# Optimization experiments

Hardware: AMD Instinct MI355X
Metric: run time of the kernel (lower is better)

The kernel has to match this reference:

```python
import jax, jax.numpy as jnp
import numpy as np

H = 2048       # hidden_size
E = 8          # num_experts
K = 2          # top_k
I = 16         # expert bottleneck (intermediate_size)


def setup_inputs() -> dict:
    key = jax.random.key(0)
    k1, k2, k3, k4 = jax.random.split(key, 4)
    B, T = 2, 4096
    x = jax.random.normal(k1, (B, T, H), dtype=jnp.float32)
    # nn.Linear weight layout is (out, in); init scale ~ 1/sqrt(fan_in)
    router_w = jax.random.normal(k2, (E, H), dtype=jnp.float32) / np.sqrt(H)
    down_w = jax.random.normal(k3, (E, I, H), dtype=jnp.float32) / np.sqrt(H)
    up_w = jax.random.normal(k4, (E, H, I), dtype=jnp.float32) / np.sqrt(I)
    return {"x": x, "router_w": router_w, "down_w": down_w, "up_w": up_w}


def reference(x, router_w, down_w, up_w):
    # router
    logits = jnp.einsum('bth,eh->bte', x, router_w)        # [B,T,E]
    weights = jax.nn.softmax(logits, axis=-1)
    top_w, top_idx = jax.lax.top_k(weights, K)             # [B,T,K]
    # gate[b,t,e] = softmax weight if e in top-k else 0 (top-k of softmax
    # values are distinct a.s., so masking == scatter of top_w)
    topk_mask = jnp.sum(jax.nn.one_hot(top_idx, E, dtype=x.dtype), axis=-2)  # [B,T,E]
    gate = weights * topk_mask                              # [B,T,E]
    # dense expert compute on all tokens (matches original's redundant compute)
    h = jnp.einsum('bth,eih->beti', x, down_w)             # [B,E,T,I]
    a = jax.nn.silu(h)
    expert_out = jnp.einsum('beti,ehi->beth', a, up_w)     # [B,E,T,H]
    # masked combine
    out = jnp.einsum('beth,bte->bth', expert_out, gate)    # [B,T,H]
    return out
```

## Files before the change

kernel.cpp:

```cpp
#include <hip/hip_runtime.h>
#include <math.h>

#define HDIM 2048
#define NEXP 8
#define IDIM 16
#define N_EI 128

typedef __attribute__((ext_vector_type(8))) short bf16x8;
typedef __attribute__((ext_vector_type(4))) float f32x4;

static __device__ __forceinline__ short f2bf(float f) {
    union { float f; unsigned u; } v; v.f = f;
    unsigned r = v.u + 0x7fffu + ((v.u >> 16) & 1u);
    return (short)(r >> 16);
}

__global__ __launch_bounds__(256) void prep_kernel(
    const float* __restrict__ x, const float* __restrict__ rw,
    const float* __restrict__ dw, const float* __restrict__ uw,
    float* __restrict__ gate_ws, short* __restrict__ b1p, short* __restrict__ b2p,
    short* __restrict__ x_bf, int T, int routerBlocks, int doXbf)
{
    const int bid = blockIdx.x;
    if (bid < routerBlocks) {
        const int wave = threadIdx.x >> 6, lane = threadIdx.x & 63;
        const int t = bid * 4 + wave;
        const float* __restrict__ xr = x + (size_t)t * HDIM;
        float4 xv[8];
        #pragma unroll
        for (int j = 0; j < 8; ++j) xv[j] = *(const float4*)(xr + j * 256 + lane * 4);

        if (doXbf) {
            #pragma unroll
            for (int j = 0; j < 8; ++j) {
                unsigned lo = ((unsigned short)f2bf(xv[j].x)) | ((unsigned)(unsigned short)f2bf(xv[j].y) << 16);
                unsigned hi = ((unsigned short)f2bf(xv[j].z)) | ((unsigned)(unsigned short)f2bf(xv[j].w) << 16);
                *(uint2*)(x_bf + (size_t)t * HDIM + j * 256 + lane * 4) = make_uint2(lo, hi);
            }
        }

        float accv[NEXP];
        #pragma unroll
        for (int e = 0; e < NEXP; ++e) {
            const float* __restrict__ wr = rw + (size_t)e * HDIM;
            float acc = 0.f;
            #pragma unroll
            for (int j = 0; j < 8; ++j) {
                float4 wv = *(const float4*)(wr + j * 256 + lane * 4);
                acc += xv[j].x * wv.x + xv[j].y * wv.y + xv[j].z * wv.z + xv[j].w * wv.w;
            }
            accv[e] = acc;
        }
        #pragma unroll
        for (int s = 1; s < 64; s <<= 1) {
            #pragma unroll
            for (int e = 0; e < NEXP; ++e) accv[e] += __shfl_xor(accv[e], s);
        }
        if (lane == 0) {
            float m = accv[0];
            #pragma unroll
            for (int e = 1; e < NEXP; ++e) m = fmaxf(m, accv[e]);
            float w[NEXP], ssum = 0.f;
            #pragma unroll
            for (int e = 0; e < NEXP; ++e) { w[e] = expf(accv[e] - m); ssum += w[e]; }
            const float inv = 1.f / ssum;
            #pragma unroll
            for (int e = 0; e < NEXP; ++e) w[e] *= inv;
            int i1 = 0; float w1 = w[0];
            #pragma unroll
            for (int e = 1; e < NEXP; ++e) if (w[e] > w1) { w1 = w[e]; i1 = e; }
            int i2 = -1; float w2 = -1.f;
            #pragma unroll
            for (int e = 0; e < NEXP; ++e) if (e != i1 && w[e] > w2) { w2 = w[e]; i2 = e; }
            #pragma unroll
            for (int e = 0; e < NEXP; ++e)
                gate_ws[(size_t)t * NEXP + e] = (e == i1) ? w1 : ((e == i2) ? w2 : 0.f);
        }
    } else {
        const int id = (bid - routerBlocks) * 256 + threadIdx.x;
        float4 v0, v1;
        short* dst;
        if (id < 32768) {
            const int kb = id >> 7, n = id & 127;
            const float* __restrict__ src = dw + (size_t)n * HDIM + kb * 8;
            v0 = *(const float4*)(src);
            v1 = *(const float4*)(src + 4);
            dst = b1p + (size_t)id * 8;
        } else {
            const int id2 = id - 32768;
            const int k2b = id2 >> 11, h = id2 & 2047;
            const int e = k2b >> 1, i0 = (k2b & 1) * 8;
            const float* __restrict__ src = uw + ((size_t)e * HDIM + h) * IDIM + i0;
            v0 = *(const float4*)(src);
            v1 = *(const float4*)(src + 4);
            dst = b2p + (size_t)id2 * 8;
        }
        bf16x8 p;
        p[0] = f2bf(v0.x); p[1] = f2bf(v0.y); p[2] = f2bf(v0.z); p[3] = f2bf(v0.w);
        p[4] = f2bf(v1.x); p[5] = f2bf(v1.y); p[6] = f2bf(v1.z); p[7] = f2bf(v1.w);
        *(bf16x8*)dst = p;
    }
}

template<bool XBF>
__global__ __launch_bounds__(512) void down_kernel(
    const float* __restrict__ x, const short* __restrict__ x_bf,
    const float* __restrict__ gate_ws, const short* __restrict__ b1p,
    short* __restrict__ a_gl, int T)
{
    __shared__ float h_part[16][132];

    const int tid = threadIdx.x;
    const int w = tid >> 6, l = tid & 63;
    const int c = l & 15;
    const int kblk = l >> 4;
    const int t0 = blockIdx.x * 16;
    const int nq = w & 3, kh = w >> 2;
    const int n0 = nq * 32;

    f32x4 acc0 = {0,0,0,0}, acc1 = {0,0,0,0};
    const float* __restrict__ xr = x + (size_t)(t0 + c) * HDIM;
    const short* __restrict__ xb = x_bf + (size_t)(t0 + c) * HDIM;

    for (int s = 0; s < 32; ++s) {
        const int k0 = kh * 1024 + s * 32;
        const int ka = k0 + kblk * 8;
        bf16x8 xf;
        if (XBF) {
            xf = *(const bf16x8*)(xb + ka);
        } else {
            float4 a0 = *(const float4*)(xr + ka);
            float4 a1 = *(const float4*)(xr + ka + 4);
            xf[0]=f2bf(a0.x); xf[1]=f2bf(a0.y); xf[2]=f2bf(a0.z); xf[3]=f2bf(a0.w);
            xf[4]=f2bf(a1.x); xf[5]=f2bf(a1.y); xf[6]=f2bf(a1.z); xf[7]=f2bf(a1.w);
        }
        const short* __restrict__ bbase = b1p + ((size_t)(k0 >> 3) + kblk) * 1024;
        bf16x8 wf0 = *(const bf16x8*)(bbase + (n0 + c) * 8);
        bf16x8 wf1 = *(const bf16x8*)(bbase + (n0 + 16 + c) * 8);
        acc0 = __builtin_amdgcn_mfma_f32_16x16x32_bf16(wf0, xf, acc0, 0, 0, 0);
        acc1 = __builtin_amdgcn_mfma_f32_16x16x32_bf16(wf1, xf, acc1, 0, 0, 0);
    }

    if (kh == 1) {
        *(f32x4*)&h_part[c][n0 + kblk * 4]      = acc0;
        *(f32x4*)&h_part[c][n0 + 16 + kblk * 4] = acc1;
    }
    __syncthreads();
    if (kh == 0) {
        const f32x4 pa = *(const f32x4*)&h_part[c][n0 + kblk * 4];
        const f32x4 pb = *(const f32x4*)&h_part[c][n0 + 16 + kblk * 4];
        const float g0 = gate_ws[(size_t)(t0 + c) * NEXP + nq * 2];
        const float g1 = gate_ws[(size_t)(t0 + c) * NEXP + nq * 2 + 1];
        short r0[4], r1[4];
        #pragma unroll
        for (int r = 0; r < 4; ++r) {
            const float h0v = acc0[r] + pa[r];
            const float h1v = acc1[r] + pb[r];
            r0[r] = f2bf(h0v / (1.f + expf(-h0v)) * g0);
            r1[r] = f2bf(h1v / (1.f + expf(-h1v)) * g1);
        }
        short* __restrict__ arow = a_gl + (size_t)(t0 + c) * N_EI;
        *(uint2*)(arow + n0 + kblk * 4) =
            make_uint2(((unsigned short)r0[0]) | ((unsigned)(unsigned short)r0[1] << 16),
                       ((unsigned short)r0[2]) | ((unsigned)(unsigned short)r0[3] << 16));
        *(uint2*)(arow + n0 + 16 + kblk * 4) =
            make_uint2(((unsigned short)r1[0]) | ((unsigned)(unsigned short)r1[1] << 16),
                       ((unsigned short)r1[2]) | ((unsigned)(unsigned short)r1[3] << 16));
    }
}

__global__ __launch_bounds__(512) void up_kernel(
    const short* __restrict__ a_gl, const short* __restrict__ b2p,
    float* __restrict__ out, int T)
{
    const int tid = threadIdx.x;
    const int w = tid >> 6, l = tid & 63;
    const int c = l & 15;
    const int kblk = l >> 4;
    const int bid = blockIdx.x;
    const int tgrp = bid >> 1, bh = bid & 1;
    const int th = w >> 2, hq = w & 3;
    const int t0 = tgrp * 32 + th * 16;
    const int h0 = bh * 1024 + hq * 256;

    f32x4 acc[16];
    #pragma unroll
    for (int f = 0; f < 16; ++f) acc[f] = (f32x4){0,0,0,0};

    const short* __restrict__ arow = a_gl + (size_t)(t0 + c) * N_EI;
    for (int s = 0; s < 4; ++s) {
        bf16x8 af = *(const bf16x8*)(arow + s * 32 + kblk * 8);
        const short* __restrict__ bbase = b2p + ((size_t)(s * 4) + kblk) * 16384;
        #pragma unroll
        for (int f = 0; f < 16; ++f) {
            bf16x8 wfr = *(const bf16x8*)(bbase + (size_t)(h0 + f * 16 + c) * 8);
            acc[f] = __builtin_amdgcn_mfma_f32_16x16x32_bf16(wfr, af, acc[f], 0, 0, 0);
        }
    }
    float* __restrict__ orow = out + (size_t)(t0 + c) * HDIM;
    #pragma unroll
    for (int f = 0; f < 16; ++f)
        *(f32x4*)(orow + h0 + f * 16 + kblk * 4) = acc[f];
}

extern "C" void kernel_launch(void* const* d_in, const int* in_sizes, int n_in,
                              void* d_out, int out_size, void* d_ws, size_t ws_size,
                              hipStream_t stream) {
    const float* x  = (const float*)d_in[0];
    const float* rw = (const float*)d_in[1];
    const float* dw = (const float*)d_in[2];
    const float* uw = (const float*)d_in[3];
    float* out = (float*)d_out;
    const int T = in_sizes[0] / HDIM;

    char* wsb = (char*)d_ws;
    float* gate_ws = (float*)wsb;
    short* b1p  = (short*)(wsb + (size_t)T * NEXP * 4);
    short* b2p  = (short*)(wsb + (size_t)T * NEXP * 4 + 524288);
    short* x_bf = (short*)(wsb + (size_t)T * NEXP * 4 + 1048576);
    const size_t xbf_bytes = (size_t)T * HDIM * 2;

    const size_t need_full  = (size_t)T * NEXP * 4 + 1048576 + xbf_bytes + (size_t)T * N_EI * 2;
    const bool use_xbf = (ws_size >= need_full);
    short* a_gl = use_xbf
        ? (short*)(wsb + (size_t)T * NEXP * 4 + 1048576 + xbf_bytes)
        : (short*)(wsb + (size_t)T * NEXP * 4 + 1048576);

    const int routerBlocks = T / 4;
    prep_kernel<<<routerBlocks + 256, 256, 0, stream>>>(
        x, rw, dw, uw, gate_ws, b1p, b2p, x_bf, T, routerBlocks, use_xbf ? 1 : 0);

    if (use_xbf)
        down_kernel<true><<<T / 16, 512, 0, stream>>>(x, x_bf, gate_ws, b1p, a_gl, T);
    else
        down_kernel<false><<<T / 16, 512, 0, stream>>>(x, x_bf, gate_ws, b1p, a_gl, T);

    up_kernel<<<(T / 32) * 2, 512, 0, stream>>>(a_gl, b2p, out, T);
}
```

Baseline: 173.1 us.

## Fuse router logits, softmax and top-k gating into the down-projection kernel

The router dot products are now computed inside the down-projection kernel from the fp32 x values it already loads, so x is read once instead of twice. The separate bf16 copy of x is no longer written, and the gates stay in LDS instead of going through global memory. Weight packing becomes a small standalone kernel. In exchange the down kernel takes extra router-weight loads, LDS reductions and two more barriers, and every block repeats the weight packing work's dependency order.

```diff
diff --git a/kernel.cpp b/kernel.cpp
--- a/kernel.cpp
+++ b/kernel.cpp
@@ -15,100 +15,42 @@
     return (short)(r >> 16);
 }
 
-__global__ __launch_bounds__(256) void prep_kernel(
+__global__ __launch_bounds__(256) void pack_kernel(
+    const float* __restrict__ dw, const float* __restrict__ uw,
+    short* __restrict__ b1p, short* __restrict__ b2p)
+{
+    const int id = blockIdx.x * 256 + threadIdx.x;
+    float4 v0, v1;
+    short* dst;
+    if (id < 32768) {
+        const int kb = id >> 7, n = id & 127;
+        const float* __restrict__ src = dw + (size_t)n * HDIM + kb * 8;
+        v0 = *(const float4*)(src);
+        v1 = *(const float4*)(src + 4);
+        dst = b1p + (size_t)id * 8;
+    } else {
+        const int id2 = id - 32768;
+        const int k2b = id2 >> 11, h = id2 & 2047;
+        const int e = k2b >> 1, i0 = (k2b & 1) * 8;
+        const float* __restrict__ src = uw + ((size_t)e * HDIM + h) * IDIM + i0;
+        v0 = *(const float4*)(src);
+        v1 = *(const float4*)(src + 4);
+        dst = b2p + (size_t)id2 * 8;
+    }
+    bf16x8 p;
+    p[0] = f2bf(v0.x); p[1] = f2bf(v0.y); p[2] = f2bf(v0.z); p[3] = f2bf(v0.w);
+    p[4] = f2bf(v1.x); p[5] = f2bf(v1.y); p[6] = f2bf(v1.z); p[7] = f2bf(v1.w);
+    *(bf16x8*)dst = p;
+}
+
+__global__ __launch_bounds__(512) void downr_kernel(
     const float* __restrict__ x, const float* __restrict__ rw,
-    const float* __restrict__ dw, const float* __restrict__ uw,
-    float* __restrict__ gate_ws, short* __restrict__ b1p, short* __restrict__ b2p,
-    short* __restrict__ x_bf, int T, int routerBlocks, int doXbf)
-{
-    const int bid = blockIdx.x;
-    if (bid < routerBlocks) {
-        const int wave = threadIdx.x >> 6, lane = threadIdx.x & 63;
-        const int t = bid * 4 + wave;
-        const float* __restrict__ xr = x + (size_t)t * HDIM;
-        float4 xv[8];
-        #pragma unroll
-        for (int j = 0; j < 8; ++j) xv[j] = *(const float4*)(xr + j * 256 + lane * 4);
-
-        if (doXbf) {
-            #pragma unroll
-            for (int j = 0; j < 8; ++j) {
-                unsigned lo = ((unsigned short)f2bf(xv[j].x)) | ((unsigned)(unsigned short)f2bf(xv[j].y) << 16);
-                unsigned hi = ((unsigned short)f2bf(xv[j].z)) | ((unsigned)(unsigned short)f2bf(xv[j].w) << 16);
-                *(uint2*)(x_bf + (size_t)t * HDIM + j * 256 + lane * 4) = make_uint2(lo, hi);
-            }
-        }
-
-        float accv[NEXP];
-        #pragma unroll
-        for (int e = 0; e < NEXP; ++e) {
-            const float* __restrict__ wr = rw + (size_t)e * HDIM;
-            float acc = 0.f;
-            #pragma unroll
-            for (int j = 0; j < 8; ++j) {
-                float4 wv = *(const float4*)(wr + j * 256 + lane * 4);
-                acc += xv[j].x * wv.x + xv[j].y * wv.y + xv[j].z * wv.z + xv[j].w * wv.w;
-            }
-            accv[e] = acc;
-        }
-        #pragma unroll
-        for (int s = 1; s < 64; s <<= 1) {
-            #pragma unroll
-            for (int e = 0; e < NEXP; ++e) accv[e] += __shfl_xor(accv[e], s);
-        }
-        if (lane == 0) {
-            float m = accv[0];
-            #pragma unroll
-            for (int e = 1; e < NEXP; ++e) m = fmaxf(m, accv[e]);
-            float w[NEXP], ssum = 0.f;
-            #pragma unroll
-            for (int e = 0; e < NEXP; ++e) { w[e] = expf(accv[e] - m); ssum += w[e]; }
-            const float inv = 1.f / ssum;
-            #pragma unroll
-            for (int e = 0; e < NEXP; ++e) w[e] *= inv;
-            int i1 = 0; float w1 = w[0];
-            #pragma unroll
-            for (int e = 1; e < NEXP; ++e) if (w[e] > w1) { w1 = w[e]; i1 = e; }
-            int i2 = -1; float w2 = -1.f;
-            #pragma unroll
-            for (int e = 0; e < NEXP; ++e) if (e != i1 && w[e] > w2) { w2 = w[e]; i2 = e; }
-            #pragma unroll
-            for (int e = 0; e < NEXP; ++e)
-                gate_ws[(size_t)t * NEXP + e] = (e == i1) ? w1 : ((e == i2) ? w2 : 0.f);
-        }
-    } else {
-        const int id = (bid - routerBlocks) * 256 + threadIdx.x;
-        float4 v0, v1;
-        short* dst;
-        if (id < 32768) {
-            const int kb = id >> 7, n = id & 127;
-            const float* __restrict__ src = dw + (size_t)n * HDIM + kb * 8;
-            v0 = *(const float4*)(src);
-            v1 = *(const float4*)(src + 4);
-            dst = b1p + (size_t)id * 8;
-        } else {
-            const int id2 = id - 32768;
-            const int k2b = id2 >> 11, h = id2 & 2047;
-            const int e = k2b >> 1, i0 = (k2b & 1) * 8;
-            const float* __restrict__ src = uw + ((size_t)e * HDIM + h) * IDIM + i0;
-            v0 = *(const float4*)(src);
-            v1 = *(const float4*)(src + 4);
-            dst = b2p + (size_t)id2 * 8;
-        }
-        bf16x8 p;
-        p[0] = f2bf(v0.x); p[1] = f2bf(v0.y); p[2] = f2bf(v0.z); p[3] = f2bf(v0.w);
-        p[4] = f2bf(v1.x); p[5] = f2bf(v1.y); p[6] = f2bf(v1.z); p[7] = f2bf(v1.w);
-        *(bf16x8*)dst = p;
-    }
-}
-
-template<bool XBF>
-__global__ __launch_bounds__(512) void down_kernel(
-    const float* __restrict__ x, const short* __restrict__ x_bf,
-    const float* __restrict__ gate_ws, const short* __restrict__ b1p,
-    short* __restrict__ a_gl, int T)
+    const short* __restrict__ b1p, short* __restrict__ a_gl, int T)
 {
     __shared__ float h_part[16][132];
+    __shared__ float lp[32][16][8];
+    __shared__ float logit2[16][8];
+    __shared__ float gate_lds[16][8];
 
     const int tid = threadIdx.x;
     const int w = tid >> 6, l = tid & 63;
@@ -119,38 +61,87 @@
     const int n0 = nq * 32;
 
     f32x4 acc0 = {0,0,0,0}, acc1 = {0,0,0,0};
+    float accR[NEXP];
+    #pragma unroll
+    for (int e = 0; e < NEXP; ++e) accR[e] = 0.f;
+
     const float* __restrict__ xr = x + (size_t)(t0 + c) * HDIM;
-    const short* __restrict__ xb = x_bf + (size_t)(t0 + c) * HDIM;
-
+
+    #pragma unroll 8
     for (int s = 0; s < 32; ++s) {
         const int k0 = kh * 1024 + s * 32;
         const int ka = k0 + kblk * 8;
+        float4 a0 = *(const float4*)(xr + ka);
+        float4 a1 = *(const float4*)(xr + ka + 4);
         bf16x8 xf;
-        if (XBF) {
-            xf = *(const bf16x8*)(xb + ka);
-        } else {
-            float4 a0 = *(const float4*)(xr + ka);
-            float4 a1 = *(const float4*)(xr + ka + 4);
-            xf[0]=f2bf(a0.x); xf[1]=f2bf(a0.y); xf[2]=f2bf(a0.z); xf[3]=f2bf(a0.w);
-            xf[4]=f2bf(a1.x); xf[5]=f2bf(a1.y); xf[6]=f2bf(a1.z); xf[7]=f2bf(a1.w);
-        }
+        xf[0]=f2bf(a0.x); xf[1]=f2bf(a0.y); xf[2]=f2bf(a0.z); xf[3]=f2bf(a0.w);
+        xf[4]=f2bf(a1.x); xf[5]=f2bf(a1.y); xf[6]=f2bf(a1.z); xf[7]=f2bf(a1.w);
         const short* __restrict__ bbase = b1p + ((size_t)(k0 >> 3) + kblk) * 1024;
         bf16x8 wf0 = *(const bf16x8*)(bbase + (n0 + c) * 8);
         bf16x8 wf1 = *(const bf16x8*)(bbase + (n0 + 16 + c) * 8);
         acc0 = __builtin_amdgcn_mfma_f32_16x16x32_bf16(wf0, xf, acc0, 0, 0, 0);
         acc1 = __builtin_amdgcn_mfma_f32_16x16x32_bf16(wf1, xf, acc1, 0, 0, 0);
-    }
-
+        if ((s >> 3) == nq) {
+            #pragma unroll
+            for (int e = 0; e < NEXP; ++e) {
+                const float* __restrict__ wr = rw + (size_t)e * HDIM + ka;
+                float4 w0 = *(const float4*)(wr);
+                float4 w1 = *(const float4*)(wr + 4);
+                accR[e] += a0.x*w0.x + a0.y*w0.y + a0.z*w0.z + a0.w*w0.w
+                         + a1.x*w1.x + a1.y*w1.y + a1.z*w1.z + a1.w*w1.w;
+            }
+        }
+    }
+
+    {
+        f32x4 ra = {accR[0], accR[1], accR[2], accR[3]};
+        f32x4 rb = {accR[4], accR[5], accR[6], accR[7]};
+        *(f32x4*)&lp[(w << 2) | kblk][c][0] = ra;
+        *(f32x4*)&lp[(w << 2) | kblk][c][4] = rb;
+    }
     if (kh == 1) {
         *(f32x4*)&h_part[c][n0 + kblk * 4]      = acc0;
         *(f32x4*)&h_part[c][n0 + 16 + kblk * 4] = acc1;
     }
     __syncthreads();
+
+    if (tid < 128) {
+        const int t = tid >> 3, e = tid & 7;
+        float s = 0.f;
+        #pragma unroll
+        for (int sl = 0; sl < 32; ++sl) s += lp[sl][t][e];
+        logit2[t][e] = s;
+    }
+    __syncthreads();
+
+    if (tid < 16) {
+        float wv[NEXP];
+        float m = logit2[tid][0];
+        #pragma unroll
+        for (int e = 1; e < NEXP; ++e) m = fmaxf(m, logit2[tid][e]);
+        float ssum = 0.f;
+        #pragma unroll
+        for (int e = 0; e < NEXP; ++e) { wv[e] = expf(logit2[tid][e] - m); ssum += wv[e]; }
+        const float inv = 1.f / ssum;
+        #pragma unroll
+        for (int e = 0; e < NEXP; ++e) wv[e] *= inv;
+        int i1 = 0; float w1 = wv[0];
+        #pragma unroll
+        for (int e = 1; e < NEXP; ++e) if (wv[e] > w1) { w1 = wv[e]; i1 = e; }
+        int i2 = -1; float w2 = -1.f;
+        #pragma unroll
+        for (int e = 0; e < NEXP; ++e) if (e != i1 && wv[e] > w2) { w2 = wv[e]; i2 = e; }
+        #pragma unroll
+        for (int e = 0; e < NEXP; ++e)
+            gate_lds[tid][e] = (e == i1) ? w1 : ((e == i2) ? w2 : 0.f);
+    }
+    __syncthreads();
+
     if (kh == 0) {
         const f32x4 pa = *(const f32x4*)&h_part[c][n0 + kblk * 4];
         const f32x4 pb = *(const f32x4*)&h_part[c][n0 + 16 + kblk * 4];
-        const float g0 = gate_ws[(size_t)(t0 + c) * NEXP + nq * 2];
-        const float g1 = gate_ws[(size_t)(t0 + c) * NEXP + nq * 2 + 1];
+        const float g0 = gate_lds[c][nq * 2];
+        const float g1 = gate_lds[c][nq * 2 + 1];
         short r0[4], r1[4];
         #pragma unroll
         for (int r = 0; r < 4; ++r) {
@@ -214,26 +205,11 @@
     const int T = in_sizes[0] / HDIM;
 
     char* wsb = (char*)d_ws;
-    float* gate_ws = (float*)wsb;
-    short* b1p  = (short*)(wsb + (size_t)T * NEXP * 4);
-    short* b2p  = (short*)(wsb + (size_t)T * NEXP * 4 + 524288);
-    short* x_bf = (short*)(wsb + (size_t)T * NEXP * 4 + 1048576);
-    const size_t xbf_bytes = (size_t)T * HDIM * 2;
-
-    const size_t need_full  = (size_t)T * NEXP * 4 + 1048576 + xbf_bytes + (size_t)T * N_EI * 2;
-    const bool use_xbf = (ws_size >= need_full);
-    short* a_gl = use_xbf
-        ? (short*)(wsb + (size_t)T * NEXP * 4 + 1048576 + xbf_bytes)
-        : (short*)(wsb + (size_t)T * NEXP * 4 + 1048576);
-
-    const int routerBlocks = T / 4;
-    prep_kernel<<<routerBlocks + 256, 256, 0, stream>>>(
-        x, rw, dw, uw, gate_ws, b1p, b2p, x_bf, T, routerBlocks, use_xbf ? 1 : 0);
-
-    if (use_xbf)
-        down_kernel<true><<<T / 16, 512, 0, stream>>>(x, x_bf, gate_ws, b1p, a_gl, T);
-    else
-        down_kernel<false><<<T / 16, 512, 0, stream>>>(x, x_bf, gate_ws, b1p, a_gl, T);
-
+    short* b1p  = (short*)wsb;
+    short* b2p  = (short*)(wsb + 524288);
+    short* a_gl = (short*)(wsb + 1048576);
+
+    pack_kernel<<<256, 256, 0, stream>>>(dw, uw, b1p, b2p);
+    downr_kernel<<<T / 16, 512, 0, stream>>>(x, rw, b1p, a_gl, T);
     up_kernel<<<(T / 32) * 2, 512, 0, stream>>>(a_gl, b2p, out, T);
 }
```

Measured after the change: 179.8 us. +3.9%, slower.
